# Kernel optimization log

Hardware: AMD Instinct MI355X
Metric: run time of the kernel (lower is better)

Reference implementation:

```python
import jax, jax.numpy as jnp
import numpy as np

E, S, H, D, B = 8, 64, 2048, 1024, 8192
LN_EPS = 1e-5


def setup_inputs() -> dict:
    key = jax.random.key(0)
    ks = jax.random.split(key, 12)
    n = lambda k, shape: jax.random.normal(k, shape, jnp.float32) * 0.02
    return {
        "raw_state": jax.random.normal(ks[0], (B, S), jnp.float32),
        "has_proprio": jax.random.randint(ks[1], (B,), 0, 2, jnp.int32),
        "expert_idx": jax.random.randint(ks[2], (B,), 0, E, jnp.int32),
        "pw1": n(ks[3], (E, S, H)), "pb1": jnp.zeros((E, H), jnp.float32),
        "pw2": n(ks[4], (E, H, D)), "pb2": jnp.zeros((E, D), jnp.float32),
        "qw1": n(ks[5], (E, S, H)), "qb1": jnp.zeros((E, H), jnp.float32),
        "qw2": n(ks[6], (E, H, D)), "qb2": jnp.zeros((E, D), jnp.float32),
        "ln_g": jnp.ones((E, D), jnp.float32), "ln_b": jnp.zeros((E, D), jnp.float32),
        "tw1": n(ks[7], (E, D, H)), "tb1": jnp.zeros((E, H), jnp.float32),
        "tw2": n(ks[8], (E, H, D)), "tb2": jnp.zeros((E, D), jnp.float32),
    }


def _gelu(x):
    # torch nn.GELU default = exact erf form
    return jax.nn.gelu(x, approximate=False)


def _expert_fwd(x, sel, w):
    (pw1, pb1, pw2, pb2, qw1, qb1, qw2, qb2, ln_g, ln_b, tw1, tb1, tw2, tb2) = w
    placeholder = _gelu(x @ pw1 + pb1) @ pw2 + pb2      # [B, D]
    proprio = _gelu(x @ qw1 + qb1) @ qw2 + qb2          # [B, D]
    mixed = placeholder * (1.0 - sel) + proprio * sel    # [B, D]
    mu = jnp.mean(mixed, axis=-1, keepdims=True)
    var = jnp.mean(jnp.square(mixed - mu), axis=-1, keepdims=True)
    normed = (mixed - mu) * jax.lax.rsqrt(var + LN_EPS) * ln_g + ln_b
    return _gelu(normed @ tw1 + tb1) @ tw2 + tb2         # [B, D]


def reference(raw_state, has_proprio, expert_idx,
              pw1, pb1, pw2, pb2, qw1, qb1, qw2, qb2,
              ln_g, ln_b, tw1, tb1, tw2, tb2):
    sel = has_proprio.astype(raw_state.dtype)[:, None]  # [B, 1]
    n_experts = pw1.shape[0]
    acc = jnp.zeros((raw_state.shape[0], tw2.shape[-1]), raw_state.dtype)
    # Fixed small loop over experts; rows routed via mask-select (same math
    # as the original index_select -> projector -> index_copy_).
    for e in range(n_experts):
        w = (pw1[e], pb1[e], pw2[e], pb2[e], qw1[e], qb1[e], qw2[e], qb2[e],
             ln_g[e], ln_b[e], tw1[e], tb1[e], tw2[e], tb2[e])
        oe = _expert_fwd(raw_state, sel, w)
        acc = jnp.where((expert_idx == e)[:, None], oe, acc)
    return acc[:, None, :]  # [B, 1, D]
```

## Files before the change

### kernel.cpp

```cpp
#include <hip/hip_runtime.h>
#include <math.h>

typedef unsigned short u16;
typedef unsigned int   u32;
typedef __attribute__((ext_vector_type(8))) short bh8;
typedef __attribute__((ext_vector_type(4))) float f4;

#define TM 128
#define TN 128
#define TK 32

__device__ __forceinline__ u16 f2b(float f) {
  u32 u = __builtin_bit_cast(u32, f);
  u += 0x7fffu + ((u >> 16) & 1u);
  return (u16)(u >> 16);
}
__device__ __forceinline__ float gelu_f(float x) {
  return 0.5f * x * (1.0f + erff(x * 0.70710678118654752f));
}

__device__ __forceinline__ void gl2lds16(const u16* g, u16* l) {
  __builtin_amdgcn_global_load_lds(
      (const __attribute__((address_space(1))) u32*)g,
      (__attribute__((address_space(3))) u32*)l, 16, 0, 0);
}

__global__ __launch_bounds__(128) void init_routing(int* __restrict__ R) {
  R[threadIdx.x] = 0;
}

__global__ __launch_bounds__(256) void hist_kernel(const int* __restrict__ eidx,
                                                   const int* __restrict__ hasp,
                                                   int* __restrict__ R,
                                                   int* __restrict__ grp) {
  int t = blockIdx.x * 256 + threadIdx.x;
  int g = eidx[t] * 2 + (hasp[t] != 0 ? 1 : 0);
  grp[t] = g;
  atomicAdd(&R[g], 1);
}

__global__ __launch_bounds__(64) void scan_kernel(int* __restrict__ R) {
  if (threadIdx.x == 0) {
    int* cnt = R; int* cur = R + 16; int* gs = R + 32; int* to = R + 64;
    gs[0] = 0; to[0] = 0;
    for (int g = 0; g < 16; g++) {
      gs[g + 1] = gs[g] + cnt[g];
      cur[g] = gs[g];
      to[g + 1] = to[g] + (cnt[g] + TM - 1) / TM;
    }
  }
}

__global__ __launch_bounds__(256) void scatter_kernel(const int* __restrict__ grp,
                                                      int* __restrict__ R,
                                                      int* __restrict__ perm) {
  int t = blockIdx.x * 256 + threadIdx.x;
  int g = grp[t];
  int pos = atomicAdd(&R[16 + g], 1);
  perm[pos] = t;
}

__global__ __launch_bounds__(256) void gather_kernel(const float* __restrict__ raw,
                                                     const int* __restrict__ perm,
                                                     u16* __restrict__ Xg) {
  int t = blockIdx.x * 256 + threadIdx.x;
  int pos = t >> 6, ln = t & 63;
  int orig = perm[pos];
  Xg[(size_t)pos * 64 + ln] = f2b(raw[(size_t)orig * 64 + ln]);
}

__global__ __launch_bounds__(256) void transpose_cvt(const float* __restrict__ srcP,
                                                     const float* __restrict__ srcQ,
                                                     int twoSrc, int Rr, int Cc,
                                                     u16* __restrict__ dst) {
  int m = blockIdx.z;
  const float* src = twoSrc ? (((m & 1) ? srcQ : srcP) + (size_t)(m >> 1) * Rr * Cc)
                            : (srcP + (size_t)m * Rr * Cc);
  u16* d = dst + (size_t)m * Rr * Cc;
  __shared__ u16 t[64][66];
  int c0 = blockIdx.x * 64, r0 = blockIdx.y * 64;
  int tx = threadIdx.x, ty = threadIdx.y;
#pragma unroll
  for (int i = 0; i < 16; i++) {
    int r = ty + i * 4;
    t[tx][r] = f2b(src[(size_t)(r0 + r) * Cc + c0 + tx]);
  }
  __syncthreads();
#pragma unroll
  for (int i = 0; i < 16; i++) {
    int c = ty + i * 4;
    d[(size_t)(c0 + c) * Rr + r0 + tx] = t[c][tx];
  }
}

__global__ __launch_bounds__(256)
void gemm_grouped(const u16* __restrict__ A, int lda,
                  const u16* __restrict__ W, int wShift, int K, int N,
                  const float* __restrict__ biasP, const float* __restrict__ biasQ,
                  int branchBias, int doGelu,
                  u16* __restrict__ outB, float* __restrict__ outF,
                  int doScatter, int ldo,
                  const int* __restrict__ gstart, const int* __restrict__ tileOff,
                  const int* __restrict__ perm) {
  __shared__ __align__(16) u16 As[TM * TK];
  __shared__ __align__(16) u16 Bs[TN * TK];

  int bidM = blockIdx.x;
  int tot = tileOff[16];
  if (bidM >= tot) return;
  int g = 0;
  while (g < 15 && bidM >= tileOff[g + 1]) g++;
  int rowStart = gstart[g] + (bidM - tileOff[g]) * TM;
  int rowEnd = gstart[g + 1];

  const u16* Wg = W + (size_t)(g >> wShift) * N * K;
  int e = g >> 1;
  const float* bias = ((branchBias && (g & 1)) ? biasQ : biasP) + (size_t)e * N;

  int tid = threadIdx.x;
  int lane = tid & 63;
  int wv = tid >> 6;
  int wm = (wv >> 1) * 64, wn = (wv & 1) * 64;
  int l15 = lane & 15, l4 = lane >> 4;
  int colBase = blockIdx.y * TN;

  int cA = wv * 2;
  int rA0 = cA * 16 + (lane >> 2);
  int rA1 = rA0 + 16;
  int kq8 = (lane & 3) * 8;
  int grA0 = rowStart + rA0; grA0 = grA0 < rowEnd ? grA0 : (rowEnd - 1);
  int grA1 = rowStart + rA1; grA1 = grA1 < rowEnd ? grA1 : (rowEnd - 1);
  const u16* aSrc0 = A + (size_t)grA0 * lda + kq8;
  const u16* aSrc1 = A + (size_t)grA1 * lda + kq8;
  const u16* bSrc0 = Wg + (size_t)(colBase + rA0) * K + kq8;
  const u16* bSrc1 = Wg + (size_t)(colBase + rA1) * K + kq8;
  u16* aDst0 = &As[cA * 512];
  u16* aDst1 = &As[cA * 512 + 512];
  u16* bDst0 = &Bs[cA * 512];
  u16* bDst1 = &Bs[cA * 512 + 512];

  f4 acc[4][4];
#pragma unroll
  for (int i = 0; i < 4; i++)
#pragma unroll
    for (int j = 0; j < 4; j++) acc[i][j] = (f4){0.f, 0.f, 0.f, 0.f};

  for (int k0 = 0; k0 < K; k0 += TK) {
    __syncthreads();
    gl2lds16(aSrc0 + k0, aDst0);
    gl2lds16(aSrc1 + k0, aDst1);
    gl2lds16(bSrc0 + k0, bDst0);
    gl2lds16(bSrc1 + k0, bDst1);
    __syncthreads();

    bh8 a[4], b[4];
#pragma unroll
    for (int i = 0; i < 4; i++)
      a[i] = *reinterpret_cast<const bh8*>(&As[(wm + i * 16 + l15) * TK + l4 * 8]);
#pragma unroll
    for (int j = 0; j < 4; j++)
      b[j] = *reinterpret_cast<const bh8*>(&Bs[(wn + j * 16 + l15) * TK + l4 * 8]);
#pragma unroll
    for (int i = 0; i < 4; i++)
#pragma unroll
      for (int j = 0; j < 4; j++)
        acc[i][j] = __builtin_amdgcn_mfma_f32_16x16x32_bf16(a[i], b[j], acc[i][j], 0, 0, 0);
  }

#pragma unroll
  for (int i = 0; i < 4; i++) {
#pragma unroll
    for (int r = 0; r < 4; r++) {
      int row = rowStart + wm + i * 16 + l4 * 4 + r;
      if (row < rowEnd) {
        int orow = doScatter ? perm[row] : row;
#pragma unroll
        for (int j = 0; j < 4; j++) {
          int col = colBase + wn + j * 16 + l15;
          float v = acc[i][j][r] + bias[col];
          if (doGelu) v = gelu_f(v);
          if (outF) outF[(size_t)orow * ldo + col] = v;
          else      outB[(size_t)orow * ldo + col] = f2b(v);
        }
      }
    }
  }
}

__global__ __launch_bounds__(256) void ln_kernel(const float* __restrict__ MIX,
                                                 u16* __restrict__ NRM,
                                                 const float* __restrict__ lng,
                                                 const float* __restrict__ lnb,
                                                 const int* __restrict__ gstart) {
  const int D = 1024;
  int pos = blockIdx.x;
  int g = 0;
  while (g < 15 && pos >= gstart[g + 1]) g++;
  int e = g >> 1;
  int tid = threadIdx.x;
  float x[4];
  float s = 0.f, s2 = 0.f;
#pragma unroll
  for (int i = 0; i < 4; i++) {
    float v = MIX[(size_t)pos * D + tid + i * 256];
    x[i] = v; s += v; s2 += v * v;
  }
#pragma unroll
  for (int off = 32; off >= 1; off >>= 1) {
    s += __shfl_down(s, off);
    s2 += __shfl_down(s2, off);
  }
  __shared__ float red[8];
  int wv = tid >> 6;
  if ((tid & 63) == 0) { red[wv] = s; red[4 + wv] = s2; }
  __syncthreads();
  if (tid == 0) {
    red[0] = red[0] + red[1] + red[2] + red[3];
    red[4] = red[4] + red[5] + red[6] + red[7];
  }
  __syncthreads();
  float mean = red[0] / D;
  float var = red[4] / D - mean * mean;
  float rstd = rsqrtf(var + 1e-5f);
#pragma unroll
  for (int i = 0; i < 4; i++) {
    int c = tid + i * 256;
    float v = (x[i] - mean) * rstd * lng[(size_t)e * D + c] + lnb[(size_t)e * D + c];
    NRM[(size_t)pos * D + c] = f2b(v);
  }
}

extern "C" void kernel_launch(void* const* d_in, const int* in_sizes, int n_in,
                              void* d_out, int out_size, void* d_ws, size_t ws_size,
                              hipStream_t stream) {
  const float* raw = (const float*)d_in[0];
  const int* hasp = (const int*)d_in[1];
  const int* eidx = (const int*)d_in[2];
  const float* pw1 = (const float*)d_in[3];  const float* pb1 = (const float*)d_in[4];
  const float* pw2 = (const float*)d_in[5];  const float* pb2 = (const float*)d_in[6];
  const float* qw1 = (const float*)d_in[7];  const float* qb1 = (const float*)d_in[8];
  const float* qw2 = (const float*)d_in[9];  const float* qb2 = (const float*)d_in[10];
  const float* lng = (const float*)d_in[11]; const float* lnb = (const float*)d_in[12];
  const float* tw1 = (const float*)d_in[13]; const float* tb1 = (const float*)d_in[14];
  const float* tw2 = (const float*)d_in[15]; const float* tb2 = (const float*)d_in[16];
  float* out = (float*)d_out;

  const int B = in_sizes[0] / 64;
  const int S = 64, H = 2048, D = 1024, E = 8;

  char* ws = (char*)d_ws;
  size_t o = 0;
  int* R    = (int*)(ws + o); o += 1024;
  int* grp  = (int*)(ws + o); o += (size_t)B * 4;
  int* perm = (int*)(ws + o); o += (size_t)B * 4;
  u16* Xg   = (u16*)(ws + o); o += (size_t)B * S * 2;
  u16* Hbuf = (u16*)(ws + o); o += (size_t)B * H * 2;
  float* MIX = (float*)(ws + o); o += (size_t)B * D * 4;
  u16* NRM  = (u16*)(ws + o); o += (size_t)B * D * 2;
  u16* W1T  = (u16*)(ws + o); o += (size_t)2 * E * S * H * 2;
  u16* WB   = (u16*)(ws + o);
  u16* T1T  = WB;
  u16* T2T  = WB + (size_t)E * D * H;

  int* gstart = R + 32;
  int* toff = R + 64;

  init_routing<<<1, 128, 0, stream>>>(R);
  hist_kernel<<<B / 256, 256, 0, stream>>>(eidx, hasp, R, grp);
  scan_kernel<<<1, 64, 0, stream>>>(R);
  scatter_kernel<<<B / 256, 256, 0, stream>>>(grp, R, perm);
  gather_kernel<<<B / 4, 256, 0, stream>>>(raw, perm, Xg);

  dim3 tb(64, 4);
  transpose_cvt<<<dim3(H / 64, S / 64, 16), tb, 0, stream>>>(pw1, qw1, 1, S, H, W1T);
  transpose_cvt<<<dim3(D / 64, H / 64, 16), tb, 0, stream>>>(pw2, qw2, 1, H, D, WB);

  const int maxT = B / TM + 16;
  gemm_grouped<<<dim3(maxT, H / TN), 256, 0, stream>>>(
      Xg, S, W1T, 0, S, H, pb1, qb1, 1, 1, Hbuf, nullptr, 0, H, gstart, toff, perm);
  gemm_grouped<<<dim3(maxT, D / TN), 256, 0, stream>>>(
      Hbuf, H, WB, 0, H, D, pb2, qb2, 1, 0, nullptr, MIX, 0, D, gstart, toff, perm);
  ln_kernel<<<B, 256, 0, stream>>>(MIX, NRM, lng, lnb, gstart);
  transpose_cvt<<<dim3(H / 64, D / 64, 8), tb, 0, stream>>>(tw1, nullptr, 0, D, H, T1T);
  transpose_cvt<<<dim3(D / 64, H / 64, 8), tb, 0, stream>>>(tw2, nullptr, 0, H, D, T2T);
  gemm_grouped<<<dim3(maxT, H / TN), 256, 0, stream>>>(
      NRM, D, T1T, 1, D, H, tb1, nullptr, 0, 1, Hbuf, nullptr, 0, H, gstart, toff, perm);
  gemm_grouped<<<dim3(maxT, D / TN), 256, 0, stream>>>(
      Hbuf, H, T2T, 1, H, D, tb2, nullptr, 0, 0, nullptr, out, 1, D, gstart, toff, perm);
}
```

Baseline: 652.1 us.

## Double-buffer LDS tiles with TK=64 and XOR-swizzled layout in grouped GEMM

The grouped GEMM main loop now uses two LDS buffers, so global-to-LDS loads for the next K tile are issued before computing on the current one, with one barrier per iteration instead of two. The K tile doubles to 64, and LDS chunks are XOR-swizzled by row to avoid bank conflicts on the wider rows. This uses more LDS (64KB per block), which may lower occupancy, and relies on the async loads finishing before the barrier.

```diff
diff --git a/kernel.cpp b/kernel.cpp
--- a/kernel.cpp
+++ b/kernel.cpp
@@ -8,7 +8,7 @@
 
 #define TM 128
 #define TN 128
-#define TK 32
+#define TK 64
 
 __device__ __forceinline__ u16 f2b(float f) {
   u32 u = __builtin_bit_cast(u32, f);
@@ -102,8 +102,8 @@
                   int doScatter, int ldo,
                   const int* __restrict__ gstart, const int* __restrict__ tileOff,
                   const int* __restrict__ perm) {
-  __shared__ __align__(16) u16 As[TM * TK];
-  __shared__ __align__(16) u16 Bs[TN * TK];
+  __shared__ __align__(16) u16 As[2][TM * TK];
+  __shared__ __align__(16) u16 Bs[2][TN * TK];
 
   int bidM = blockIdx.x;
   int tot = tileOff[16];
@@ -124,20 +124,18 @@
   int l15 = lane & 15, l4 = lane >> 4;
   int colBase = blockIdx.y * TN;
 
-  int cA = wv * 2;
-  int rA0 = cA * 16 + (lane >> 2);
-  int rA1 = rA0 + 16;
-  int kq8 = (lane & 3) * 8;
-  int grA0 = rowStart + rA0; grA0 = grA0 < rowEnd ? grA0 : (rowEnd - 1);
-  int grA1 = rowStart + rA1; grA1 = grA1 < rowEnd ? grA1 : (rowEnd - 1);
-  const u16* aSrc0 = A + (size_t)grA0 * lda + kq8;
-  const u16* aSrc1 = A + (size_t)grA1 * lda + kq8;
-  const u16* bSrc0 = Wg + (size_t)(colBase + rA0) * K + kq8;
-  const u16* bSrc1 = Wg + (size_t)(colBase + rA1) * K + kq8;
-  u16* aDst0 = &As[cA * 512];
-  u16* aDst1 = &As[cA * 512 + 512];
-  u16* bDst0 = &Bs[cA * 512];
-  u16* bDst1 = &Bs[cA * 512 + 512];
+  int rsub = lane >> 3;
+  int schunk = (lane & 7) ^ rsub;
+  int c0 = wv * 4;
+  const u16* aSrc[4];
+  const u16* bSrc[4];
+#pragma unroll
+  for (int q = 0; q < 4; q++) {
+    int rt = (c0 + q) * 8 + rsub;
+    int ga = rowStart + rt; ga = ga < rowEnd ? ga : (rowEnd - 1);
+    aSrc[q] = A + (size_t)ga * lda + schunk * 8;
+    bSrc[q] = Wg + (size_t)(colBase + rt) * K + schunk * 8;
+  }
 
   f4 acc[4][4];
 #pragma unroll
@@ -145,27 +143,53 @@
 #pragma unroll
     for (int j = 0; j < 4; j++) acc[i][j] = (f4){0.f, 0.f, 0.f, 0.f};
 
-  for (int k0 = 0; k0 < K; k0 += TK) {
+  int rx = l15 & 7;
+  int aBase = (wm + l15) * TK;
+  int bBase = (wn + l15) * TK;
+
+#define STAGE(buf, k0)                                                        \
+  do {                                                                        \
+    _Pragma("unroll")                                                         \
+    for (int q = 0; q < 4; q++) {                                             \
+      gl2lds16(aSrc[q] + (k0), &As[(buf)][(c0 + q) * 512]);                   \
+      gl2lds16(bSrc[q] + (k0), &Bs[(buf)][(c0 + q) * 512]);                   \
+    }                                                                         \
+  } while (0)
+
+#define COMPUTE(buf)                                                          \
+  do {                                                                        \
+    _Pragma("unroll")                                                         \
+    for (int ks = 0; ks < 2; ks++) {                                          \
+      int ch = ((ks << 2) | l4) ^ rx;                                         \
+      bh8 a[4], b[4];                                                         \
+      _Pragma("unroll")                                                       \
+      for (int i = 0; i < 4; i++)                                             \
+        a[i] = *reinterpret_cast<const bh8*>(                                 \
+            &As[(buf)][aBase + i * (16 * TK) + ch * 8]);                      \
+      _Pragma("unroll")                                                       \
+      for (int j = 0; j < 4; j++)                                             \
+        b[j] = *reinterpret_cast<const bh8*>(                                 \
+            &Bs[(buf)][bBase + j * (16 * TK) + ch * 8]);                      \
+      _Pragma("unroll")                                                       \
+      for (int i = 0; i < 4; i++)                                             \
+        _Pragma("unroll")                                                     \
+        for (int j = 0; j < 4; j++)                                           \
+          acc[i][j] = __builtin_amdgcn_mfma_f32_16x16x32_bf16(                \
+              a[i], b[j], acc[i][j], 0, 0, 0);                                \
+    }                                                                         \
+  } while (0)
+
+  int nk = K / TK;
+  STAGE(0, 0);
+  __syncthreads();
+  int cur = 0;
+  for (int t = 1; t < nk; ++t) {
+    STAGE(cur ^ 1, t * TK);
+    COMPUTE(cur);
     __syncthreads();
-    gl2lds16(aSrc0 + k0, aDst0);
-    gl2lds16(aSrc1 + k0, aDst1);
-    gl2lds16(bSrc0 + k0, bDst0);
-    gl2lds16(bSrc1 + k0, bDst1);
-    __syncthreads();
-
-    bh8 a[4], b[4];
-#pragma unroll
-    for (int i = 0; i < 4; i++)
-      a[i] = *reinterpret_cast<const bh8*>(&As[(wm + i * 16 + l15) * TK + l4 * 8]);
-#pragma unroll
-    for (int j = 0; j < 4; j++)
-      b[j] = *reinterpret_cast<const bh8*>(&Bs[(wn + j * 16 + l15) * TK + l4 * 8]);
-#pragma unroll
-    for (int i = 0; i < 4; i++)
-#pragma unroll
-      for (int j = 0; j < 4; j++)
-        acc[i][j] = __builtin_amdgcn_mfma_f32_16x16x32_bf16(a[i], b[j], acc[i][j], 0, 0, 0);
-  }
+    cur ^= 1;
+  }
+  COMPUTE(cur);
 
 #pragma unroll
   for (int i = 0; i < 4; i++) {
@@ -185,6 +209,8 @@
       }
     }
   }
+#undef STAGE
+#undef COMPUTE
 }
 
 __global__ __launch_bounds__(256) void ln_kernel(const float* __restrict__ MIX,
```

Measured after the change: 719.6 us. 10.3% more time.
